# Performance work log

Hardware: AMD Instinct MI355X
Metric: run time of the kernel (lower is better)

## Reference

```python
import jax, jax.numpy as jnp
import numpy as np

D_MODEL = 1024
N_HEADS = 16
HEAD_DIM = D_MODEL // N_HEADS


def setup_inputs() -> dict:
    key = jax.random.key(0)
    ks = jax.random.split(key, 9)
    B, S = 2, 2048
    s = 1.0 / np.sqrt(D_MODEL)
    return {
        "x": jax.random.normal(ks[0], (B, S, D_MODEL), dtype=jnp.float32),
        "Wq": jax.random.normal(ks[1], (D_MODEL, D_MODEL), dtype=jnp.float32) * s,
        "bq": jnp.zeros((D_MODEL,), dtype=jnp.float32),
        "Wk": jax.random.normal(ks[2], (D_MODEL, D_MODEL), dtype=jnp.float32) * s,
        "bk": jnp.zeros((D_MODEL,), dtype=jnp.float32),
        "Wv": jax.random.normal(ks[3], (D_MODEL, D_MODEL), dtype=jnp.float32) * s,
        "bv": jnp.zeros((D_MODEL,), dtype=jnp.float32),
        "Wo": jax.random.normal(ks[4], (D_MODEL, D_MODEL), dtype=jnp.float32) * s,
        "bo": jnp.zeros((D_MODEL,), dtype=jnp.float32),
    }


def _rope_emb(seq_len, dtype):
    # inv_freq over even dims of head_dim; emb = cat(freqs, freqs)
    inv_freq = 1.0 / (10000.0 ** (jnp.arange(0, HEAD_DIM, 2, dtype=jnp.float32) / HEAD_DIM))
    t = jnp.arange(seq_len, dtype=jnp.float32)
    freqs = t[:, None] * inv_freq[None, :]          # [S, head_dim/2]
    emb = jnp.concatenate([freqs, freqs], axis=-1)  # [S, head_dim]
    return emb.astype(dtype)[None, None, :, :]       # [1,1,S,head_dim]


def _rotate_half(x):
    x1, x2 = jnp.split(x, 2, axis=-1)
    return jnp.concatenate([-x2, x1], axis=-1)


def _apply_rope(x, emb):
    return x * jnp.cos(emb) + _rotate_half(x) * jnp.sin(emb)


def reference(x, Wq, bq, Wk, bk, Wv, bv, Wo, bo):
    B, S, _ = x.shape
    # projections (torch Linear: x @ W.T + b; here W is stored already as [in,out])
    q = (x @ Wq + bq).reshape(B, S, N_HEADS, HEAD_DIM).transpose(0, 2, 1, 3)
    k = (x @ Wk + bk).reshape(B, S, N_HEADS, HEAD_DIM).transpose(0, 2, 1, 3)
    v = (x @ Wv + bv).reshape(B, S, N_HEADS, HEAD_DIM).transpose(0, 2, 1, 3)
    emb = _rope_emb(S, x.dtype)
    q = _apply_rope(q, emb)
    k = _apply_rope(k, emb)
    scores = jnp.einsum('bhqd,bhkd->bhqk', q, k) / jnp.sqrt(jnp.asarray(HEAD_DIM, x.dtype))
    attn = jax.nn.softmax(scores, axis=-1)
    out = jnp.einsum('bhqk,bhkd->bhqd', attn, v)
    out = out.transpose(0, 2, 1, 3).reshape(B, S, D_MODEL)
    return out @ Wo + bo
```

## Files before the change

### kernel.cpp

```cpp
#include <hip/hip_runtime.h>
#include <hip/hip_bf16.h>
#include <math.h>

#define SEQ 2048
#define DM 1024
#define NH 16
#define HD 64
#define NBH 32
#define MTOT 4096

typedef __attribute__((ext_vector_type(8))) short short8;
typedef __attribute__((ext_vector_type(4))) float floatx4;
typedef __attribute__((ext_vector_type(8))) unsigned short u16x8;
typedef __attribute__((ext_vector_type(4))) unsigned short u16x4;

__device__ __forceinline__ unsigned short f2bf(float f) {
    unsigned int u = __float_as_uint(f);
    u += 0x7FFFu + ((u >> 16) & 1u);
    return (unsigned short)(u >> 16);
}

#define AS1C const __attribute__((address_space(1))) void*
#define AS3  __attribute__((address_space(3))) void*

#define QSCALE 0.18033688011112042f

__global__ __launch_bounds__(256) void cvt_x_kernel(
    const float* __restrict__ x, unsigned short* __restrict__ xb)
{
    size_t base = ((size_t)blockIdx.x * 256 + threadIdx.x) * 8;
    float4 a = *(const float4*)(x + base);
    float4 b = *(const float4*)(x + base + 4);
    u16x8 o;
    o[0]=f2bf(a.x); o[1]=f2bf(a.y); o[2]=f2bf(a.z); o[3]=f2bf(a.w);
    o[4]=f2bf(b.x); o[5]=f2bf(b.y); o[6]=f2bf(b.z); o[7]=f2bf(b.w);
    *(u16x8*)(xb + base) = o;
}

__global__ __launch_bounds__(256) void cvt_w_kernel(
    const float* __restrict__ Wq, const float* __restrict__ Wk,
    const float* __restrict__ Wv, const float* __restrict__ Wo,
    unsigned short* __restrict__ Wt)
{
    __shared__ float Ls[64][65];
    const int z = blockIdx.z;
    const float* src = (z==0) ? Wq : (z==1) ? Wk : (z==2) ? Wv : Wo;
    unsigned short* dst = Wt + (size_t)z * DM * DM;
    const int tid = threadIdx.x;
    const int k0 = blockIdx.x * 64, n0 = blockIdx.y * 64;

    int r = tid >> 2, cseg = (tid & 3) * 16;
    #pragma unroll
    for (int e = 0; e < 4; ++e) {
        float4 v = *(const float4*)(src + (size_t)(k0 + r) * DM + n0 + cseg + e*4);
        Ls[r][cseg+e*4+0] = v.x; Ls[r][cseg+e*4+1] = v.y;
        Ls[r][cseg+e*4+2] = v.z; Ls[r][cseg+e*4+3] = v.w;
    }
    __syncthreads();
    int n = tid >> 2, kseg = (tid & 3) * 16;
    #pragma unroll
    for (int half = 0; half < 2; ++half) {
        u16x8 o;
        #pragma unroll
        for (int e = 0; e < 8; ++e) o[e] = f2bf(Ls[kseg + half*8 + e][n]);
        *(u16x8*)(dst + (size_t)(n0 + n) * DM + k0 + kseg + half*8) = o;
    }
}

#define GEMM_CORE(A_, Bt_, m0_, n0_)                                          \
    const int tid = threadIdx.x;                                              \
    const int wave = tid >> 6, lane = tid & 63;                               \
    const int quad = lane >> 4, l16 = lane & 15;                              \
    const int mh = (wave & 1) * 64, nh = (wave >> 1) * 64;                    \
    floatx4 acc[4][4];                                                        \
    _Pragma("unroll")                                                         \
    for (int i = 0; i < 4; ++i)                                               \
        _Pragma("unroll")                                                     \
        for (int j = 0; j < 4; ++j) acc[i][j] = (floatx4){0.f,0.f,0.f,0.f};   \
    {                                                                         \
        const int srow = wave*32 + (lane>>2);                                 \
        const int scol = (lane & 3) * 8;                                      \
        const unsigned short* ga = A_ + (size_t)(m0_ + srow)*DM + scol;       \
        const unsigned short* gb = Bt_ + (size_t)(n0_ + srow)*DM + scol;      \
        char* lA = (char*)As; char* lB = (char*)Bs;                           \
        for (int k0 = 0; k0 < DM; k0 += 32) {                                 \
            __syncthreads();                                                  \
            _Pragma("unroll")                                                 \
            for (int u = 0; u < 2; ++u) {                                     \
                __builtin_amdgcn_global_load_lds(                             \
                    (AS1C)(ga + (size_t)u*16*DM + k0),                        \
                    (AS3)(lA + (wave*32 + u*16)*64), 16, 0, 0);               \
                __builtin_amdgcn_global_load_lds(                             \
                    (AS1C)(gb + (size_t)u*16*DM + k0),                        \
                    (AS3)(lB + (wave*32 + u*16)*64), 16, 0, 0);               \
            }                                                                 \
            __syncthreads();                                                  \
            short8 af[4], bf[4];                                              \
            _Pragma("unroll")                                                 \
            for (int t = 0; t < 4; ++t) {                                     \
                af[t] = *(const short8*)&As[(mh + t*16 + l16)*32 + quad*8];   \
                bf[t] = *(const short8*)&Bs[(nh + t*16 + l16)*32 + quad*8];   \
            }                                                                 \
            _Pragma("unroll")                                                 \
            for (int mt = 0; mt < 4; ++mt)                                    \
                _Pragma("unroll")                                             \
                for (int nt = 0; nt < 4; ++nt)                                \
                    acc[mt][nt] = __builtin_amdgcn_mfma_f32_16x16x32_bf16(    \
                        af[mt], bf[nt], acc[mt][nt], 0, 0, 0);                \
        }                                                                     \
    }

__global__ __launch_bounds__(256, 3) void qkv_gemm_kernel(
    const unsigned short* __restrict__ xb, const unsigned short* __restrict__ Wt,
    const float* __restrict__ bq, const float* __restrict__ bk,
    const float* __restrict__ bv,
    unsigned short* __restrict__ qb, unsigned short* __restrict__ kb,
    unsigned short* __restrict__ vtg)
{
    __shared__ unsigned short As[128*32];
    __shared__ unsigned short Bs[128*32];
    const int z = blockIdx.z;
    const unsigned short* Bt = Wt + (size_t)z * DM * DM;
    const float* bias = (z==0) ? bq : (z==1) ? bk : bv;
    const int m0 = blockIdx.x * 128, n0 = blockIdx.y * 128;

    GEMM_CORE(xb, Bt, m0, n0)

    float bb[4];
    #pragma unroll
    for (int nt = 0; nt < 4; ++nt) bb[nt] = bias[n0 + nh + nt*16 + l16];

    if (z == 2) {
        unsigned short* Tw = (wave & 1) ? Bs : As;
        const int b = m0 >> 11;
        const int bufsel = tid >> 7, nl = tid & 127;
        const int ng = n0 + nl, hh = ng >> 6, dhh = ng & 63;
        unsigned short* vrow = vtg + ((size_t)((b*NH + hh)*HD + dhh))*SEQ;
        #pragma unroll
        for (int t = 0; t < 4; ++t) {
            __syncthreads();
            #pragma unroll
            for (int nt = 0; nt < 4; ++nt)
                #pragma unroll
                for (int r = 0; r < 4; ++r)
                    Tw[(nh + nt*16 + l16)*24 + quad*4 + r] =
                        f2bf(acc[t][nt][r] + bb[nt]);
            __syncthreads();
            const unsigned short* T2 = bufsel ? Bs : As;
            int sbase = (m0 & 2047) + bufsel*64 + t*16;
            u16x8 lo = *(const u16x8*)&T2[nl*24];
            u16x8 hi = *(const u16x8*)&T2[nl*24 + 8];
            *(u16x8*)(vrow + sbase)     = lo;
            *(u16x8*)(vrow + sbase + 8) = hi;
        }
    } else {
        unsigned short* outh = (z==0) ? qb : kb;
        const float scl = (z == 0) ? QSCALE : 1.0f;
        const int h = (n0 + nh) >> 6;
        float inv0 = __expf(-(float)l16        * 0.28782313662425572f);
        float inv1 = __expf(-(float)(l16 + 16) * 0.28782313662425572f);
        #pragma unroll
        for (int mt = 0; mt < 4; ++mt)
            #pragma unroll
            for (int r = 0; r < 4; ++r) {
                int m = m0 + mh + mt*16 + quad*4 + r;
                int b = m >> 11, s = m & (SEQ-1);
                float s0, c0, s1, c1;
                __sincosf((float)s * inv0, &s0, &c0);
                __sincosf((float)s * inv1, &s1, &c1);
                float a0 = acc[mt][0][r] + bb[0];
                float a1 = acc[mt][1][r] + bb[1];
                float a2 = acc[mt][2][r] + bb[2];
                float a3 = acc[mt][3][r] + bb[3];
                u16x4 o;
                o[0] = f2bf((a0*c0 - a2*s0) * scl);
                o[1] = f2bf((a1*c1 - a3*s1) * scl);
                o[2] = f2bf((a2*c0 + a0*s0) * scl);
                o[3] = f2bf((a3*c1 + a1*s1) * scl);
                *(u16x4*)(outh + ((size_t)((b*NH + h)*SEQ + s))*HD + 4*l16) = o;
            }
    }
}

__global__ __launch_bounds__(256, 3) void out_gemm_kernel(
    const unsigned short* __restrict__ ctxb, const unsigned short* __restrict__ Wto,
    const float* __restrict__ bo, float* __restrict__ outf)
{
    __shared__ unsigned short As[128*32];
    __shared__ unsigned short Bs[128*32];
    const int m0 = blockIdx.x * 128, n0 = blockIdx.y * 128;

    GEMM_CORE(ctxb, Wto, m0, n0)

    float bb[4];
    #pragma unroll
    for (int nt = 0; nt < 4; ++nt) bb[nt] = bo[n0 + nh + nt*16 + l16];
    #pragma unroll
    for (int mt = 0; mt < 4; ++mt)
        #pragma unroll
        for (int r = 0; r < 4; ++r) {
            int m = m0 + mh + mt*16 + quad*4 + r;
            #pragma unroll
            for (int nt = 0; nt < 4; ++nt) {
                int n = n0 + nh + nt*16 + l16;
                outf[(size_t)m*DM + n] = acc[mt][nt][r] + bb[nt];
            }
        }
}

#define LSTP 72
__global__ __launch_bounds__(512, 4) void attn_mfma_kernel(
    const unsigned short* __restrict__ Q, const unsigned short* __restrict__ K,
    const unsigned short* __restrict__ Vtg, unsigned short* __restrict__ ctxb)
{
    __shared__ unsigned short Ks[2*128*32];
    __shared__ unsigned short Vt[4*64*32];
    __shared__ unsigned short Ps[8*16*LSTP];

    const int tid  = threadIdx.x;
    const int wave = tid >> 6, lane = tid & 63;
    const int quad = lane >> 4, l16 = lane & 15;
    const int bh = blockIdx.x & 31;
    const int qt = blockIdx.x >> 5;

    const unsigned short* Qb = Q + (size_t)bh * SEQ * HD;
    const unsigned short* Kb = K + (size_t)bh * SEQ * HD;
    const unsigned short* Vb = Vtg + (size_t)bh * HD * SEQ;

    short8 qf[2];
    {
        const unsigned short* qrow = Qb + (size_t)(qt*128 + wave*16 + l16)*HD;
        qf[0] = *(const short8*)(qrow + quad*8);
        qf[1] = *(const short8*)(qrow + 32 + quad*8);
    }

    const unsigned short* gsrc[4];
    char* ldst[4];
    int step;
    {
        const int idx = (wave & 3)*64 + lane;
        if (wave < 4) {
            #pragma unroll
            for (int u = 0; u < 4; ++u) {
                int fI = u*2048 + idx*8;
                int s  = fI >> 12, rm = fI & 4095;
                int key = rm >> 5, g = ((rm >> 3) & 3) ^ (key & 3);
                gsrc[u] = Kb + (size_t)key*HD + s*32 + g*8;
                ldst[u] = (char*)Ks + (u*2048 + (wave & 3)*512)*2;
            }
            step = 128*HD;
        } else {
            #pragma unroll
            for (int u = 0; u < 4; ++u) {
                int fI = u*2048 + idx*8;
                int ch = fI >> 11, rm = fI & 2047;
                int d = rm >> 5, g = ((rm >> 3) & 3) ^ (d & 3);
                gsrc[u] = Vb + (size_t)d*SEQ + ch*32 + g*8;
                ldst[u] = (char*)Vt + (u*2048 + (wave & 3)*512)*2;
            }
            step = 128;
        }
    }

    float l_i[4];
    floatx4 Oacc[4];
    #pragma unroll
    for (int r = 0; r < 4; ++r) l_i[r] = 0.f;
    #pragma unroll
    for (int dt = 0; dt < 4; ++dt) Oacc[dt] = (floatx4){0.f,0.f,0.f,0.f};

    const int swz8 = (quad ^ (l16 & 3)) * 8;
    const int physr = ((l16 >> 2) << 1) + ((l16 & 1) << 3) + ((l16 & 2) >> 1);
    const unsigned short* parow = &Ps[(wave*16 + physr)*LSTP];
    unsigned short* pwbase = &Ps[(wave*16 + quad*2)*LSTP + l16];

    for (int kt = 0; kt < SEQ/128; ++kt) {
        __syncthreads();
        #pragma unroll
        for (int u = 0; u < 4; ++u)
            __builtin_amdgcn_global_load_lds((AS1C)gsrc[u], (AS3)ldst[u], 16, 0, 0);
        #pragma unroll
        for (int u = 0; u < 4; ++u) gsrc[u] += step;
        __syncthreads();

        floatx4 Sacc[8];
        #pragma unroll
        for (int c = 0; c < 8; ++c) Sacc[c] = (floatx4){0.f,0.f,0.f,0.f};
        #pragma unroll
        for (int s = 0; s < 2; ++s) {
            #pragma unroll
            for (int c = 0; c < 8; ++c) {
                short8 b = *(const short8*)&Ks[s*4096 + (c*16 + l16)*32 + swz8];
                Sacc[c] = __builtin_amdgcn_mfma_f32_16x16x32_bf16(qf[s], b, Sacc[c], 0, 0, 0);
            }
        }

        #pragma unroll
        for (int h = 0; h < 2; ++h) {
            #pragma unroll
            for (int r = 0; r < 4; ++r) {
                float p0 = exp2f(Sacc[h*4+0][r]);
                float p1 = exp2f(Sacc[h*4+1][r]);
                float p2 = exp2f(Sacc[h*4+2][r]);
                float p3 = exp2f(Sacc[h*4+3][r]);
                l_i[r] += (p0 + p1) + (p2 + p3);
                __hip_bfloat162 w0 = __float22bfloat162_rn(make_float2(p0, p1));
                __hip_bfloat162 w1 = __float22bfloat162_rn(make_float2(p2, p3));
                unsigned short* prow = pwbase + (((r & 1) << 3) + (r >> 1))*LSTP;
                __builtin_memcpy(&prow[0],  &w0.x, 2);
                __builtin_memcpy(&prow[16], &w0.y, 2);
                __builtin_memcpy(&prow[32], &w1.x, 2);
                __builtin_memcpy(&prow[48], &w1.y, 2);
            }
            #pragma unroll
            for (int s = 0; s < 2; ++s) {
                short8 a = *(const short8*)(parow + s*32 + quad*8);
                #pragma unroll
                for (int dt = 0; dt < 4; ++dt) {
                    short8 b = *(const short8*)&Vt[(h*2+s)*2048 + (dt*16+l16)*32 + swz8];
                    Oacc[dt] = __builtin_amdgcn_mfma_f32_16x16x32_bf16(a, b, Oacc[dt], 0, 0, 0);
                }
            }
        }
    }

    #pragma unroll
    for (int mask = 1; mask < 16; mask <<= 1)
        #pragma unroll
        for (int r = 0; r < 4; ++r)
            l_i[r] += __shfl_xor(l_i[r], mask);

    int b = bh >> 4, h = bh & 15;
    #pragma unroll
    for (int r = 0; r < 4; ++r) {
        int sr = qt*128 + wave*16 + quad*4 + r;
        float invl = 1.0f / l_i[r];
        unsigned short* dst = ctxb + ((size_t)(b*SEQ + sr))*DM + h*HD;
        #pragma unroll
        for (int dt = 0; dt < 4; ++dt)
            dst[dt*16 + l16] = f2bf(Oacc[dt][r] * invl);
    }
}

extern "C" void kernel_launch(void* const* d_in, const int* in_sizes, int n_in,
                              void* d_out, int out_size, void* d_ws, size_t ws_size,
                              hipStream_t stream) {
    const float* x  = (const float*)d_in[0];
    const float* Wq = (const float*)d_in[1];
    const float* bq = (const float*)d_in[2];
    const float* Wk = (const float*)d_in[3];
    const float* bk = (const float*)d_in[4];
    const float* Wv = (const float*)d_in[5];
    const float* bv = (const float*)d_in[6];
    const float* Wo = (const float*)d_in[7];
    const float* bo = (const float*)d_in[8];
    float* out = (float*)d_out;

    char* ws = (char*)d_ws;
    unsigned short* xb   = (unsigned short*)(ws);
    unsigned short* Wt   = (unsigned short*)(ws +  8u*1024*1024);
    unsigned short* qb   = (unsigned short*)(ws + 16u*1024*1024);
    unsigned short* kb   = (unsigned short*)(ws + 24u*1024*1024);
    unsigned short* vtg  = (unsigned short*)(ws + 32u*1024*1024);
    unsigned short* ctxb = (unsigned short*)(ws + 40u*1024*1024);

    cvt_x_kernel<<<(MTOT*DM/8)/256, 256, 0, stream>>>(x, xb);
    cvt_w_kernel<<<dim3(DM/64, DM/64, 4), 256, 0, stream>>>(Wq, Wk, Wv, Wo, Wt);

    qkv_gemm_kernel<<<dim3(MTOT/128, DM/128, 3), 256, 0, stream>>>(
        xb, Wt, bq, bk, bv, qb, kb, vtg);

    attn_mfma_kernel<<<512, 512, 0, stream>>>(qb, kb, vtg, ctxb);

    out_gemm_kernel<<<dim3(MTOT/128, DM/128), 256, 0, stream>>>(
        ctxb, Wt + (size_t)3*DM*DM, bo, out);
    (void)in_sizes; (void)n_in; (void)out_size; (void)ws_size;
}
```

Measured before the change: 212.0 us.

## Compute transposed scores so P stays in registers, halving attention block size

Result: faster. 206.1 us (-2.8%).

```diff
diff --git a/kernel.cpp b/kernel.cpp
--- a/kernel.cpp
+++ b/kernel.cpp
@@ -148,10 +148,13 @@
             __syncthreads();
             const unsigned short* T2 = bufsel ? Bs : As;
             int sbase = (m0 & 2047) + bufsel*64 + t*16;
-            u16x8 lo = *(const u16x8*)&T2[nl*24];
-            u16x8 hi = *(const u16x8*)&T2[nl*24 + 8];
-            *(u16x8*)(vrow + sbase)     = lo;
-            *(u16x8*)(vrow + sbase + 8) = hi;
+            int t32 = (sbase >> 4) & 1;
+            int sb32 = sbase & ~31;
+            #pragma unroll
+            for (int gq = 0; gq < 4; ++gq) {
+                u16x4 v4 = *(const u16x4*)&T2[nl*24 + gq*4];
+                *(u16x4*)(vrow + sb32 + gq*8 + t32*4) = v4;
+            }
         }
     } else {
         unsigned short* outh = (z==0) ? qb : kb;
@@ -208,14 +211,13 @@
         }
 }
 
-#define LSTP 72
-__global__ __launch_bounds__(512, 4) void attn_mfma_kernel(
+__global__ __launch_bounds__(256, 2) void attn_mfma_kernel(
     const unsigned short* __restrict__ Q, const unsigned short* __restrict__ K,
     const unsigned short* __restrict__ Vtg, unsigned short* __restrict__ ctxb)
 {
     __shared__ unsigned short Ks[2*128*32];
     __shared__ unsigned short Vt[4*64*32];
-    __shared__ unsigned short Ps[8*16*LSTP];
+    __shared__ float Lred[4][32];
 
     const int tid  = threadIdx.x;
     const int wave = tid >> 6, lane = tid & 63;
@@ -227,119 +229,124 @@
     const unsigned short* Kb = K + (size_t)bh * SEQ * HD;
     const unsigned short* Vb = Vtg + (size_t)bh * HD * SEQ;
 
-    short8 qf[2];
-    {
-        const unsigned short* qrow = Qb + (size_t)(qt*128 + wave*16 + l16)*HD;
-        qf[0] = *(const short8*)(qrow + quad*8);
-        qf[1] = *(const short8*)(qrow + 32 + quad*8);
-    }
-
-    const unsigned short* gsrc[4];
-    char* ldst[4];
+    short8 qf[2][2];
+    #pragma unroll
+    for (int qg = 0; qg < 2; ++qg) {
+        const unsigned short* qrow =
+            Qb + (size_t)(qt*128 + wave*32 + qg*16 + l16)*HD;
+        qf[qg][0] = *(const short8*)(qrow + quad*8);
+        qf[qg][1] = *(const short8*)(qrow + 32 + quad*8);
+    }
+
+    const unsigned short* gsrc[8];
+    char* ldst[8];
     int step;
-    {
-        const int idx = (wave & 3)*64 + lane;
-        if (wave < 4) {
-            #pragma unroll
-            for (int u = 0; u < 4; ++u) {
-                int fI = u*2048 + idx*8;
-                int s  = fI >> 12, rm = fI & 4095;
-                int key = rm >> 5, g = ((rm >> 3) & 3) ^ (key & 3);
-                gsrc[u] = Kb + (size_t)key*HD + s*32 + g*8;
-                ldst[u] = (char*)Ks + (u*2048 + (wave & 3)*512)*2;
-            }
-            step = 128*HD;
-        } else {
-            #pragma unroll
-            for (int u = 0; u < 4; ++u) {
-                int fI = u*2048 + idx*8;
-                int ch = fI >> 11, rm = fI & 2047;
-                int d = rm >> 5, g = ((rm >> 3) & 3) ^ (d & 3);
-                gsrc[u] = Vb + (size_t)d*SEQ + ch*32 + g*8;
-                ldst[u] = (char*)Vt + (u*2048 + (wave & 3)*512)*2;
-            }
-            step = 128;
-        }
-    }
-
-    float l_i[4];
-    floatx4 Oacc[4];
-    #pragma unroll
-    for (int r = 0; r < 4; ++r) l_i[r] = 0.f;
-    #pragma unroll
-    for (int dt = 0; dt < 4; ++dt) Oacc[dt] = (floatx4){0.f,0.f,0.f,0.f};
-
-    const int swz8 = (quad ^ (l16 & 3)) * 8;
-    const int physr = ((l16 >> 2) << 1) + ((l16 & 1) << 3) + ((l16 & 2) >> 1);
-    const unsigned short* parow = &Ps[(wave*16 + physr)*LSTP];
-    unsigned short* pwbase = &Ps[(wave*16 + quad*2)*LSTP + l16];
+    if (wave < 2) {
+        #pragma unroll
+        for (int u = 0; u < 8; ++u) {
+            int G = u*128 + wave*64 + lane;
+            int gl = G & 3, key = (G >> 2) & 127, s = G >> 9;
+            gsrc[u] = Kb + (size_t)key*HD + s*32 + (gl ^ ((key>>2)&3))*8;
+            ldst[u] = (char*)Ks + G*16;
+        }
+        step = 128*HD;
+    } else {
+        #pragma unroll
+        for (int u = 0; u < 8; ++u) {
+            int G = u*128 + (wave-2)*64 + lane;
+            int gl = G & 3, d = (G >> 2) & 63, g = G >> 8;
+            gsrc[u] = Vb + (size_t)d*SEQ + g*32 + (gl ^ ((d>>2)&3))*8;
+            ldst[u] = (char*)Vt + G*16;
+        }
+        step = 128;
+    }
+
+    float l_p[2] = {0.f, 0.f};
+    floatx4 Oacc[2][4];
+    #pragma unroll
+    for (int qg = 0; qg < 2; ++qg)
+        #pragma unroll
+        for (int dt = 0; dt < 4; ++dt) Oacc[qg][dt] = (floatx4){0.f,0.f,0.f,0.f};
+
+    const int swz = (quad ^ (l16 >> 2)) * 8;
 
     for (int kt = 0; kt < SEQ/128; ++kt) {
         __syncthreads();
         #pragma unroll
-        for (int u = 0; u < 4; ++u)
+        for (int u = 0; u < 8; ++u)
             __builtin_amdgcn_global_load_lds((AS1C)gsrc[u], (AS3)ldst[u], 16, 0, 0);
         #pragma unroll
-        for (int u = 0; u < 4; ++u) gsrc[u] += step;
+        for (int u = 0; u < 8; ++u) gsrc[u] += step;
         __syncthreads();
 
-        floatx4 Sacc[8];
-        #pragma unroll
-        for (int c = 0; c < 8; ++c) Sacc[c] = (floatx4){0.f,0.f,0.f,0.f};
-        #pragma unroll
-        for (int s = 0; s < 2; ++s) {
-            #pragma unroll
-            for (int c = 0; c < 8; ++c) {
-                short8 b = *(const short8*)&Ks[s*4096 + (c*16 + l16)*32 + swz8];
-                Sacc[c] = __builtin_amdgcn_mfma_f32_16x16x32_bf16(qf[s], b, Sacc[c], 0, 0, 0);
-            }
-        }
-
-        #pragma unroll
-        for (int h = 0; h < 2; ++h) {
-            #pragma unroll
-            for (int r = 0; r < 4; ++r) {
-                float p0 = exp2f(Sacc[h*4+0][r]);
-                float p1 = exp2f(Sacc[h*4+1][r]);
-                float p2 = exp2f(Sacc[h*4+2][r]);
-                float p3 = exp2f(Sacc[h*4+3][r]);
-                l_i[r] += (p0 + p1) + (p2 + p3);
-                __hip_bfloat162 w0 = __float22bfloat162_rn(make_float2(p0, p1));
-                __hip_bfloat162 w1 = __float22bfloat162_rn(make_float2(p2, p3));
-                unsigned short* prow = pwbase + (((r & 1) << 3) + (r >> 1))*LSTP;
-                __builtin_memcpy(&prow[0],  &w0.x, 2);
-                __builtin_memcpy(&prow[16], &w0.y, 2);
-                __builtin_memcpy(&prow[32], &w1.x, 2);
-                __builtin_memcpy(&prow[48], &w1.y, 2);
-            }
-            #pragma unroll
-            for (int s = 0; s < 2; ++s) {
-                short8 a = *(const short8*)(parow + s*32 + quad*8);
-                #pragma unroll
-                for (int dt = 0; dt < 4; ++dt) {
-                    short8 b = *(const short8*)&Vt[(h*2+s)*2048 + (dt*16+l16)*32 + swz8];
-                    Oacc[dt] = __builtin_amdgcn_mfma_f32_16x16x32_bf16(a, b, Oacc[dt], 0, 0, 0);
+        #pragma unroll
+        for (int g = 0; g < 4; ++g) {
+            floatx4 Sc[2][2];
+            #pragma unroll
+            for (int t = 0; t < 2; ++t)
+                #pragma unroll
+                for (int qg = 0; qg < 2; ++qg) Sc[t][qg] = (floatx4){0.f,0.f,0.f,0.f};
+            #pragma unroll
+            for (int t = 0; t < 2; ++t) {
+                const int c = g*2 + t;
+                #pragma unroll
+                for (int s = 0; s < 2; ++s) {
+                    short8 af = *(const short8*)&Ks[s*4096 + (c*16 + l16)*32 + swz];
+                    #pragma unroll
+                    for (int qg = 0; qg < 2; ++qg)
+                        Sc[t][qg] = __builtin_amdgcn_mfma_f32_16x16x32_bf16(
+                            af, qf[qg][s], Sc[t][qg], 0, 0, 0);
                 }
             }
-        }
-    }
-
-    #pragma unroll
-    for (int mask = 1; mask < 16; mask <<= 1)
-        #pragma unroll
-        for (int r = 0; r < 4; ++r)
-            l_i[r] += __shfl_xor(l_i[r], mask);
+            short8 a8[2];
+            #pragma unroll
+            for (int qg = 0; qg < 2; ++qg) {
+                float p[8];
+                #pragma unroll
+                for (int t = 0; t < 2; ++t)
+                    #pragma unroll
+                    for (int r = 0; r < 4; ++r) p[t*4+r] = exp2f(Sc[t][qg][r]);
+                l_p[qg] += ((p[0]+p[1]) + (p[2]+p[3])) + ((p[4]+p[5]) + (p[6]+p[7]));
+                u16x8 av;
+                #pragma unroll
+                for (int e = 0; e < 4; ++e) {
+                    __hip_bfloat162 w = __float22bfloat162_rn(make_float2(p[2*e], p[2*e+1]));
+                    unsigned int uu; __builtin_memcpy(&uu, &w, 4);
+                    av[2*e]   = (unsigned short)(uu & 0xFFFF);
+                    av[2*e+1] = (unsigned short)(uu >> 16);
+                }
+                __builtin_memcpy(&a8[qg], &av, 16);
+            }
+            #pragma unroll
+            for (int dt = 0; dt < 4; ++dt) {
+                short8 bf = *(const short8*)&Vt[g*2048 + (dt*16 + l16)*32 + swz];
+                #pragma unroll
+                for (int qg = 0; qg < 2; ++qg)
+                    Oacc[qg][dt] = __builtin_amdgcn_mfma_f32_16x16x32_bf16(
+                        a8[qg], bf, Oacc[qg][dt], 0, 0, 0);
+            }
+        }
+    }
+
+    #pragma unroll
+    for (int qg = 0; qg < 2; ++qg) {
+        l_p[qg] += __shfl_xor(l_p[qg], 16);
+        l_p[qg] += __shfl_xor(l_p[qg], 32);
+        Lred[wave][qg*16 + l16] = l_p[qg];
+    }
 
     int b = bh >> 4, h = bh & 15;
     #pragma unroll
-    for (int r = 0; r < 4; ++r) {
-        int sr = qt*128 + wave*16 + quad*4 + r;
-        float invl = 1.0f / l_i[r];
-        unsigned short* dst = ctxb + ((size_t)(b*SEQ + sr))*DM + h*HD;
-        #pragma unroll
-        for (int dt = 0; dt < 4; ++dt)
-            dst[dt*16 + l16] = f2bf(Oacc[dt][r] * invl);
-    }
+    for (int qg = 0; qg < 2; ++qg)
+        #pragma unroll
+        for (int r = 0; r < 4; ++r) {
+            int sr = qt*128 + wave*32 + qg*16 + quad*4 + r;
+            float invl = 1.0f / Lred[wave][qg*16 + quad*4 + r];
+            unsigned short* dst = ctxb + ((size_t)(b*SEQ + sr))*DM + h*HD;
+            #pragma unroll
+            for (int dt = 0; dt < 4; ++dt)
+                dst[dt*16 + l16] = f2bf(Oacc[qg][dt][r] * invl);
+        }
 }
 
 extern "C" void kernel_launch(void* const* d_in, const int* in_sizes, int n_in,
@@ -370,7 +377,7 @@
     qkv_gemm_kernel<<<dim3(MTOT/128, DM/128, 3), 256, 0, stream>>>(
         xb, Wt, bq, bk, bv, qb, kb, vtg);
 
-    attn_mfma_kernel<<<512, 512, 0, stream>>>(qb, kb, vtg, ctxb);
+    attn_mfma_kernel<<<512, 256, 0, stream>>>(qb, kb, vtg, ctxb);
 
     out_gemm_kernel<<<dim3(MTOT/128, DM/128), 256, 0, stream>>>(
         ctxb, Wt + (size_t)3*DM*DM, bo, out);
```
